# Kernel optimization log

Hardware: AMD Instinct MI355X
Metric: run time of the kernel (lower is better)

## Reference

```python
import jax, jax.numpy as jnp
import numpy as np

N_NODES = 100000
N_EDGES = 1600000
IN_F, HID_F, OUT_F = 128, 128, 128


def setup_inputs() -> dict:
    key = jax.random.key(0)
    ks = jax.random.split(key, 12)
    x = jax.random.normal(ks[0], (N_NODES, IN_F), dtype=jnp.float32)
    src = jax.random.randint(ks[1], (N_EDGES,), 0, N_NODES)
    dst = jax.random.randint(ks[2], (N_EDGES,), 0, N_NODES)
    s = 1.0 / np.sqrt(IN_F)
    W1_self = jax.random.uniform(ks[3], (HID_F, IN_F), minval=-s, maxval=s)
    W1_neigh = jax.random.uniform(ks[4], (HID_F, IN_F), minval=-s, maxval=s)
    b1 = jnp.zeros((HID_F,), jnp.float32)
    s2 = 1.0 / np.sqrt(HID_F)
    W2_self = jax.random.uniform(ks[5], (OUT_F, HID_F), minval=-s2, maxval=s2)
    W2_neigh = jax.random.uniform(ks[6], (OUT_F, HID_F), minval=-s2, maxval=s2)
    b2 = jnp.zeros((OUT_F,), jnp.float32)
    s3 = 1.0 / np.sqrt(OUT_F)
    W3 = jax.random.uniform(ks[7], (OUT_F, OUT_F), minval=-s3, maxval=s3)
    b3 = jax.random.uniform(ks[8], (OUT_F,), minval=-s3, maxval=s3)
    return {"x": x, "src": src, "dst": dst,
            "W1_self": W1_self, "W1_neigh": W1_neigh, "b1": b1,
            "W2_self": W2_self, "W2_neigh": W2_neigh, "b2": b2,
            "W3": W3, "b3": b3}


def _sage_conv(h, src, dst, W_self, W_neigh, b):
    # DGL SAGEConv 'mean': h_neigh = mean over in-neighbors (src -> dst)
    msg = h[src]  # [E, d] irregular gather
    summed = jax.ops.segment_sum(msg, dst, num_segments=N_NODES)  # [N, d]
    deg = jax.ops.segment_sum(jnp.ones((src.shape[0],), h.dtype), dst,
                              num_segments=N_NODES)
    h_neigh = summed / jnp.clip(deg, 1.0)[:, None]
    return h @ W_self.T + h_neigh @ W_neigh.T + b


def reference(x, src, dst, W1_self, W1_neigh, b1, W2_self, W2_neigh, b2, W3, b3):
    h = _sage_conv(x, src, dst, W1_self, W1_neigh, b1)
    h = jax.nn.relu(h)
    h = _sage_conv(h, src, dst, W2_self, W2_neigh, b2)
    return h @ W3.T + b3
```

## Files before the change

### kernel.cpp

```cpp
#include <hip/hip_runtime.h>

#define N_NODES 100000
#define N_EDGES 1600000
#define F 128
#define NB_SCAN ((N_NODES + 1023) / 1024)
#define NSUB 32
#define SUB_NODES (N_NODES / NSUB)
#define BCAP 128
#define PCAP 65536
#define NCHUNK 8
#define NCVT ((N_NODES * F / 8 + 255) / 256)
#define BUCKET_BLOCKS 512
#define PREP_BLOCKS (NCVT + 257)

typedef short short8 __attribute__((ext_vector_type(8)));
typedef float f32x4 __attribute__((ext_vector_type(4)));
typedef unsigned short ushort_t;
typedef ushort_t ushort8 __attribute__((ext_vector_type(8)));

__device__ __forceinline__ ushort_t f2b(float f) {
    union { float f; unsigned u; } v; v.f = f;
    unsigned r = v.u + 0x7fff + ((v.u >> 16) & 1);
    return (ushort_t)(r >> 16);
}


__global__ __launch_bounds__(256) void k_bucket_prep(
        const int* __restrict__ src, const int* __restrict__ dst,
        int2* __restrict__ pairs, int* __restrict__ gcur,
        const float* __restrict__ x, ushort_t* __restrict__ xb,
        const float* __restrict__ W1s, const float* __restrict__ W1n,
        const float* __restrict__ W2s, const float* __restrict__ W2n,
        const float* __restrict__ W3, const float* __restrict__ b2,
        const float* __restrict__ b3,
        ushort_t* __restrict__ wb, float* __restrict__ bc) {
    const int tid = threadIdx.x;

    if (blockIdx.x >= BUCKET_BLOCKS) {
        const int blk = blockIdx.x - BUCKET_BLOCKS;
        if (blk < NCVT) {
            int i = blk * 256 + tid;
            if (i >= N_NODES * F / 8) return;
            const float4* p = reinterpret_cast<const float4*>(x) + (size_t)i * 2;
            float4 a = p[0], b = p[1];
            ushort8 r;
            r[0] = f2b(a.x); r[1] = f2b(a.y); r[2] = f2b(a.z); r[3] = f2b(a.w);
            r[4] = f2b(b.x); r[5] = f2b(b.y); r[6] = f2b(b.z); r[7] = f2b(b.w);
            *reinterpret_cast<ushort8*>(xb + (size_t)i * 8) = r;
            return;
        }
        const int b = blk - NCVT;
        if (b < 128) {
            int g = b * 256 + tid;
            float v = (g < F * F) ? W1s[g] : W1n[g - F * F];
            wb[g] = f2b(v);
        } else if (b < 256) {
            int g = (b - 128) * 256 + tid;
            int m = g >> 14, rem = g & 16383, i = rem >> 7, j = rem & 127;
            const float* __restrict__ W2 = m ? W2n : W2s;
            float s = 0.f;
#pragma unroll 8
            for (int k = 0; k < F; ++k) s += W3[i * F + k] * W2[k * F + j];
            wb[2 * F * F + g] = f2b(s);
        } else if (tid < F) {
            float s = b3[tid];
#pragma unroll 8
            for (int k = 0; k < F; ++k) s += W3[tid * F + k] * b2[k];
            bc[tid] = s;
        }
        return;
    }

    __shared__ int2 lbuf[NSUB * BCAP];
    __shared__ int lcnt[NSUB], fbase[NSUB], fcnt[NSUB];
    if (tid < NSUB) lcnt[tid] = 0;
    __syncthreads();

    for (int base = blockIdx.x * 1024; base < N_EDGES; base += BUCKET_BLOCKS * 1024) {
#pragma unroll
        for (int r = 0; r < 4; ++r) {
            int idx = base + r * 256 + tid;
            if (idx < N_EDGES) {
                int d = dst[idx], s = src[idx];
                int p = d / SUB_NODES;
                int dl = d - p * SUB_NODES;
                int slot = atomicAdd(&lcnt[p], 1);
                if (slot < BCAP) lbuf[p * BCAP + slot] = make_int2(dl, s);
                else {
                    int g = atomicAdd(&gcur[p], 1);
                    pairs[(size_t)p * PCAP + g] = make_int2(dl, s);
                }
            }
        }
        __syncthreads();
        if (tid < NSUB) {
            int c = lcnt[tid]; if (c > BCAP) c = BCAP;
            fcnt[tid] = c;
            fbase[tid] = atomicAdd(&gcur[tid], c);
        }
        __syncthreads();
        for (int p = 0; p < NSUB; ++p) {
            int c = fcnt[p];
            for (int i = tid; i < c; i += 256)
                pairs[(size_t)p * PCAP + fbase[p] + i] = lbuf[p * BCAP + i];
        }
        __syncthreads();
        if (tid < NSUB) lcnt[tid] = 0;
        __syncthreads();
    }
}

__global__ __launch_bounds__(1024) void k_histc(const int2* __restrict__ pairs,
                                                const int* __restrict__ gcur,
                                                int* __restrict__ hists) {
    __shared__ int hc[SUB_NODES];
    const int p = blockIdx.x / NCHUNK;
    const int c = blockIdx.x % NCHUNK;
    for (int i = threadIdx.x; i < SUB_NODES; i += 1024) hc[i] = 0;
    __syncthreads();
    const int n = gcur[p];
    const int chunk = (n + NCHUNK - 1) / NCHUNK;
    const int lo = c * chunk;
    int hi = lo + chunk; if (hi > n) hi = n;
    const int2* __restrict__ sl = pairs + (size_t)p * PCAP;
    for (int i = lo + threadIdx.x; i < hi; i += 1024) atomicAdd(&hc[sl[i].x], 1);
    __syncthreads();
    int* __restrict__ hout = hists + ((size_t)p * NCHUNK + c) * SUB_NODES;
    for (int i = threadIdx.x; i < SUB_NODES; i += 1024) hout[i] = hc[i];
}

__global__ __launch_bounds__(1024) void k_scan1(const int* __restrict__ hists,
                                                int* __restrict__ tmp,
                                                int* __restrict__ bsum) {
    __shared__ int ws[16];
    const int t = threadIdx.x, lane = t & 63, w = t >> 6;
    const int gid = blockIdx.x * 1024 + t;
    int v = 0;
    if (gid < N_NODES) {
        int p = gid / SUB_NODES, i = gid - p * SUB_NODES;
        const int* __restrict__ hp = hists + (size_t)p * NCHUNK * SUB_NODES + i;
#pragma unroll
        for (int c = 0; c < NCHUNK; ++c) v += hp[c * SUB_NODES];
    }
    int x = v;
#pragma unroll
    for (int off = 1; off < 64; off <<= 1) {
        int y = __shfl_up(x, off, 64);
        if (lane >= off) x += y;
    }
    if (lane == 63) ws[w] = x;
    __syncthreads();
    if (w == 0) {
        int s = (lane < 16) ? ws[lane] : 0;
#pragma unroll
        for (int off = 1; off < 16; off <<= 1) {
            int y = __shfl_up(s, off, 64);
            if (lane >= off) s += y;
        }
        if (lane < 16) ws[lane] = s;
    }
    __syncthreads();
    int base = (w == 0) ? 0 : ws[w - 1];
    int incl = base + x;
    if (gid < N_NODES) tmp[gid] = incl;
    if (t == 1023) bsum[blockIdx.x] = incl;
}

__global__ __launch_bounds__(256) void k_scan23(const int* __restrict__ tmp,
                                                const int* __restrict__ bsum,
                                                int* __restrict__ row_ptr) {
    __shared__ int excl[NB_SCAN];
    const int t = threadIdx.x;
    if (t < 64) {
        const int lane = t;
        int v0 = (lane < NB_SCAN) ? bsum[lane] : 0;
        int v1 = (64 + lane < NB_SCAN) ? bsum[64 + lane] : 0;
        int x0 = v0;
#pragma unroll
        for (int off = 1; off < 64; off <<= 1) {
            int y = __shfl_up(x0, off, 64);
            if (lane >= off) x0 += y;
        }
        int tot0 = __shfl(x0, 63, 64);
        int x1 = v1;
#pragma unroll
        for (int off = 1; off < 64; off <<= 1) {
            int y = __shfl_up(x1, off, 64);
            if (lane >= off) x1 += y;
        }
        if (lane < NB_SCAN) excl[lane] = x0 - v0;
        if (64 + lane < NB_SCAN) excl[64 + lane] = tot0 + x1 - v1;
    }
    __syncthreads();
    int gid = blockIdx.x * 256 + t;
    if (gid >= N_NODES) return;
    row_ptr[gid + 1] = excl[gid >> 10] + tmp[gid];
    if (gid == 0) row_ptr[0] = 0;
}

__global__ __launch_bounds__(1024) void k_place2(const int2* __restrict__ pairs,
                                                 const int* __restrict__ gcur,
                                                 const int* __restrict__ row_ptr,
                                                 const int* __restrict__ hists,
                                                 int* __restrict__ col) {
    __shared__ int cur[SUB_NODES];
    const int p = blockIdx.x / NCHUNK;
    const int c = blockIdx.x % NCHUNK;
    const int* __restrict__ hp = hists + (size_t)p * NCHUNK * SUB_NODES;
    for (int i = threadIdx.x; i < SUB_NODES; i += 1024) {
        int s = row_ptr[p * SUB_NODES + i];
        for (int cc = 0; cc < c; ++cc) s += hp[cc * SUB_NODES + i];
        cur[i] = s;
    }
    __syncthreads();
    const int n = gcur[p];
    const int chunk = (n + NCHUNK - 1) / NCHUNK;
    const int lo = c * chunk;
    int hi = lo + chunk; if (hi > n) hi = n;
    const int2* __restrict__ sl = pairs + (size_t)p * PCAP;
    for (int i = lo + threadIdx.x; i < hi; i += 1024) {
        int2 pr = sl[i];
        int pos = atomicAdd(&cur[pr.x], 1);
        col[pos] = pr.y;
    }
}


__global__ __launch_bounds__(256) void k_agg(const ushort_t* __restrict__ h,
                                             const int* __restrict__ row_ptr,
                                             const int* __restrict__ col,
                                             ushort_t* __restrict__ out) {
    int node = (blockIdx.x * blockDim.x + threadIdx.x) >> 6;
    if (node >= N_NODES) return;
    const int lane = threadIdx.x & 63;
    const unsigned loff = (unsigned)lane * 4u;
    const char* __restrict__ hb = reinterpret_cast<const char*>(h);
    const int beg = row_ptr[node], end = row_ptr[node + 1];
    float ax = 0.f, ay = 0.f;
    for (int e = beg; e < end; e += 8) {
        unsigned v[8];
#pragma unroll
        for (int u = 0; u < 8; ++u) {
            int idx = e + u; idx = (idx < end) ? idx : end - 1;
            unsigned s = (unsigned)col[idx];
            v[u] = *reinterpret_cast<const unsigned*>(hb + (size_t)((s << 8) + loff));
        }
#pragma unroll
        for (int u = 0; u < 8; ++u) {
            unsigned vv = (e + u < end) ? v[u] : 0u;
            ax += __uint_as_float(vv << 16);
            ay += __uint_as_float(vv & 0xffff0000u);
        }
    }
    int deg = end - beg;
    float inv = 1.0f / (float)(deg > 0 ? deg : 1);
    unsigned r = ((unsigned)f2b(ax * inv)) | (((unsigned)f2b(ay * inv)) << 16);
    *reinterpret_cast<unsigned*>(out + ((size_t)node << 7) + lane * 2) = r;
}


template <bool RELU, bool F32OUT>
__global__ __launch_bounds__(512) void k_layer(
        const ushort_t* __restrict__ A0, const ushort_t* __restrict__ A1,
        const ushort_t* __restrict__ W0, const ushort_t* __restrict__ W1,
        const float* __restrict__ bias, void* __restrict__ outv) {
    const int t = threadIdx.x;
    const int lane = t & 63;
    const int wid = t >> 6;
    const int wr = wid >> 2;
    const int wc = wid & 3;
    const int node0 = blockIdx.x * 128;
    const int arow = lane & 15;
    const int kgrp = lane >> 4;

    f32x4 acc[4][2];
#pragma unroll
    for (int fr = 0; fr < 4; ++fr)
#pragma unroll
        for (int fc = 0; fc < 2; ++fc) acc[fr][fc] = (f32x4)(0.f);

#pragma unroll
    for (int ph = 0; ph < 2; ++ph) {
        const ushort_t* __restrict__ A = ph ? A1 : A0;
        const ushort_t* __restrict__ W = ph ? W1 : W0;

        short8 bfrag[4][2];
#pragma unroll
        for (int ks = 0; ks < 4; ++ks)
#pragma unroll
            for (int fc = 0; fc < 2; ++fc) {
                int c = wc * 32 + fc * 16 + arow;
                bfrag[ks][fc] = *reinterpret_cast<const short8*>(W + c * F + ks * 32 + kgrp * 8);
            }

#pragma unroll
        for (int ks = 0; ks < 4; ++ks) {
            short8 afrag[4];
#pragma unroll
            for (int fr = 0; fr < 4; ++fr) {
                int r = node0 + wr * 64 + fr * 16 + arow;
                if (r > N_NODES - 1) r = N_NODES - 1;
                afrag[fr] = *reinterpret_cast<const short8*>(A + (size_t)r * F + ks * 32 + kgrp * 8);
            }
#pragma unroll
            for (int fr = 0; fr < 4; ++fr)
#pragma unroll
                for (int fc = 0; fc < 2; ++fc)
                    acc[fr][fc] = __builtin_amdgcn_mfma_f32_16x16x32_bf16(
                        afrag[fr], bfrag[ks][fc], acc[fr][fc], 0, 0, 0);
        }
    }

#pragma unroll
    for (int fr = 0; fr < 4; ++fr)
#pragma unroll
        for (int fc = 0; fc < 2; ++fc) {
            int c = wc * 32 + fc * 16 + (lane & 15);
            float bv = bias[c];
#pragma unroll
            for (int r4 = 0; r4 < 4; ++r4) {
                int row = node0 + wr * 64 + fr * 16 + (lane >> 4) * 4 + r4;
                if (row >= N_NODES) continue;
                float v = acc[fr][fc][r4] + bv;
                if (RELU) v = fmaxf(v, 0.f);
                if (F32OUT)
                    reinterpret_cast<float*>(outv)[(size_t)row * F + c] = v;
                else
                    reinterpret_cast<ushort_t*>(outv)[(size_t)row * F + c] = f2b(v);
            }
        }
}


extern "C" void kernel_launch(void* const* d_in, const int* in_sizes, int n_in,
                              void* d_out, int out_size, void* d_ws, size_t ws_size,
                              hipStream_t stream) {
    const float* x   = (const float*)d_in[0];
    const int*   src = (const int*)d_in[1];
    const int*   dst = (const int*)d_in[2];
    const float* W1s = (const float*)d_in[3];
    const float* W1n = (const float*)d_in[4];
    const float* b1  = (const float*)d_in[5];
    const float* W2s = (const float*)d_in[6];
    const float* W2n = (const float*)d_in[7];
    const float* b2  = (const float*)d_in[8];
    const float* W3  = (const float*)d_in[9];
    const float* b3  = (const float*)d_in[10];
    float* out = (float*)d_out;

    char* p = (char*)d_ws;
    auto align512 = [](size_t v) { return (v + 511) & ~(size_t)511; };
    int* row_ptr = (int*)p;        p += align512((N_NODES + 1) * sizeof(int));
    int* stmp    = (int*)p;        p += align512((size_t)N_NODES * sizeof(int));
    int* bsum    = (int*)p;        p += align512(256 * sizeof(int));
    int* gcur    = (int*)p;        p += align512(NSUB * sizeof(int));
    int* col     = (int*)p;        p += align512((size_t)N_EDGES * sizeof(int));
    ushort_t* wb = (ushort_t*)p;   p += align512((size_t)4 * F * F * sizeof(ushort_t));
    float* bc    = (float*)p;      p += align512(F * sizeof(float));
    ushort_t* xb = (ushort_t*)p;   p += align512((size_t)N_NODES * F * sizeof(ushort_t));
    ushort_t* aggb = (ushort_t*)p; p += align512((size_t)N_NODES * F * sizeof(ushort_t));
    ushort_t* h1b  = (ushort_t*)p; p += align512((size_t)N_NODES * F * sizeof(ushort_t));
    int2* pairs = (int2*)aggb;
    int* hists = (int*)h1b;

    hipMemsetAsync(gcur, 0, NSUB * sizeof(int), stream);
    k_bucket_prep<<<BUCKET_BLOCKS + PREP_BLOCKS, 256, 0, stream>>>(
        src, dst, pairs, gcur, x, xb, W1s, W1n, W2s, W2n, W3, b2, b3, wb, bc);
    k_histc<<<NSUB * NCHUNK, 1024, 0, stream>>>(pairs, gcur, hists);
    k_scan1<<<NB_SCAN, 1024, 0, stream>>>(hists, stmp, bsum);
    k_scan23<<<(N_NODES + 255) / 256, 256, 0, stream>>>(stmp, bsum, row_ptr);
    k_place2<<<NSUB * NCHUNK, 1024, 0, stream>>>(pairs, gcur, row_ptr, hists, col);

    const int agg_grid = (N_NODES + 3) / 4;
    const int gemm_grid = (N_NODES + 127) / 128;

    k_agg<<<agg_grid, 256, 0, stream>>>(xb, row_ptr, col, aggb);
    k_layer<true, false><<<gemm_grid, 512, 0, stream>>>(
        xb, aggb, wb + 0 * F * F, wb + 1 * F * F, b1, h1b);

    k_agg<<<agg_grid, 256, 0, stream>>>(h1b, row_ptr, col, aggb);
    k_layer<false, true><<<gemm_grid, 512, 0, stream>>>(
        h1b, aggb, wb + 2 * F * F, wb + 3 * F * F, bc, out);
}
```

Measured before the change: 302.0 us.

## Fuse CSR scan kernels into placement kernel using per-bucket edge counts

Replaces the two global prefix-scan kernels and the separate placement kernel with one kernel. Each block gets its bucket's base offset by summing the preceding bucket counts (gcur), scans its bucket's histogram locally and then places edges. This removes two kernel launches and the intermediate temp and block-sum buffers. In exchange, every one of the NCHUNK blocks per bucket redundantly re-reads and scans the full bucket histogram.

```diff
diff --git a/kernel.cpp b/kernel.cpp
--- a/kernel.cpp
+++ b/kernel.cpp
@@ -3,7 +3,6 @@
 #define N_NODES 100000
 #define N_EDGES 1600000
 #define F 128
-#define NB_SCAN ((N_NODES + 1023) / 1024)
 #define NSUB 32
 #define SUB_NODES (N_NODES / NSUB)
 #define BCAP 128
@@ -129,20 +128,41 @@
     for (int i = threadIdx.x; i < SUB_NODES; i += 1024) hout[i] = hc[i];
 }
 
-__global__ __launch_bounds__(1024) void k_scan1(const int* __restrict__ hists,
-                                                int* __restrict__ tmp,
-                                                int* __restrict__ bsum) {
+__global__ __launch_bounds__(1024) void k_place3(const int2* __restrict__ pairs,
+                                                 const int* __restrict__ gcur,
+                                                 const int* __restrict__ hists,
+                                                 int* __restrict__ row_ptr,
+                                                 int* __restrict__ col) {
+    __shared__ int cur[SUB_NODES];
     __shared__ int ws[16];
     const int t = threadIdx.x, lane = t & 63, w = t >> 6;
-    const int gid = blockIdx.x * 1024 + t;
-    int v = 0;
-    if (gid < N_NODES) {
-        int p = gid / SUB_NODES, i = gid - p * SUB_NODES;
-        const int* __restrict__ hp = hists + (size_t)p * NCHUNK * SUB_NODES + i;
-#pragma unroll
-        for (int c = 0; c < NCHUNK; ++c) v += hp[c * SUB_NODES];
-    }
-    int x = v;
+    const int p = blockIdx.x / NCHUNK;
+    const int c = blockIdx.x % NCHUNK;
+    const int* __restrict__ hp = hists + (size_t)p * NCHUNK * SUB_NODES;
+
+    int pv = (lane < p) ? gcur[lane] : 0;
+#pragma unroll
+    for (int off = 32; off > 0; off >>= 1) pv += __shfl_xor(pv, off, 64);
+    const int pbase = pv;
+
+    int cnt[4], par[4];
+#pragma unroll
+    for (int j = 0; j < 4; ++j) {
+        int i = t * 4 + j;
+        int full = 0, part = 0;
+        if (i < SUB_NODES) {
+#pragma unroll
+            for (int cc = 0; cc < NCHUNK; ++cc) {
+                int hv = hp[cc * SUB_NODES + i];
+                full += hv;
+                if (cc < c) part += hv;
+            }
+        }
+        cnt[j] = full; par[j] = part;
+    }
+    int lsum = cnt[0] + cnt[1] + cnt[2] + cnt[3];
+
+    int x = lsum;
 #pragma unroll
     for (int off = 1; off < 64; off <<= 1) {
         int y = __shfl_up(x, off, 64);
@@ -160,65 +180,26 @@
         if (lane < 16) ws[lane] = s;
     }
     __syncthreads();
-    int base = (w == 0) ? 0 : ws[w - 1];
-    int incl = base + x;
-    if (gid < N_NODES) tmp[gid] = incl;
-    if (t == 1023) bsum[blockIdx.x] = incl;
-}
-
-__global__ __launch_bounds__(256) void k_scan23(const int* __restrict__ tmp,
-                                                const int* __restrict__ bsum,
-                                                int* __restrict__ row_ptr) {
-    __shared__ int excl[NB_SCAN];
-    const int t = threadIdx.x;
-    if (t < 64) {
-        const int lane = t;
-        int v0 = (lane < NB_SCAN) ? bsum[lane] : 0;
-        int v1 = (64 + lane < NB_SCAN) ? bsum[64 + lane] : 0;
-        int x0 = v0;
-#pragma unroll
-        for (int off = 1; off < 64; off <<= 1) {
-            int y = __shfl_up(x0, off, 64);
-            if (lane >= off) x0 += y;
-        }
-        int tot0 = __shfl(x0, 63, 64);
-        int x1 = v1;
-#pragma unroll
-        for (int off = 1; off < 64; off <<= 1) {
-            int y = __shfl_up(x1, off, 64);
-            if (lane >= off) x1 += y;
-        }
-        if (lane < NB_SCAN) excl[lane] = x0 - v0;
-        if (64 + lane < NB_SCAN) excl[64 + lane] = tot0 + x1 - v1;
-    }
-    __syncthreads();
-    int gid = blockIdx.x * 256 + t;
-    if (gid >= N_NODES) return;
-    row_ptr[gid + 1] = excl[gid >> 10] + tmp[gid];
-    if (gid == 0) row_ptr[0] = 0;
-}
-
-__global__ __launch_bounds__(1024) void k_place2(const int2* __restrict__ pairs,
-                                                 const int* __restrict__ gcur,
-                                                 const int* __restrict__ row_ptr,
-                                                 const int* __restrict__ hists,
-                                                 int* __restrict__ col) {
-    __shared__ int cur[SUB_NODES];
-    const int p = blockIdx.x / NCHUNK;
-    const int c = blockIdx.x % NCHUNK;
-    const int* __restrict__ hp = hists + (size_t)p * NCHUNK * SUB_NODES;
-    for (int i = threadIdx.x; i < SUB_NODES; i += 1024) {
-        int s = row_ptr[p * SUB_NODES + i];
-        for (int cc = 0; cc < c; ++cc) s += hp[cc * SUB_NODES + i];
-        cur[i] = s;
-    }
-    __syncthreads();
+    int run = pbase + ((w == 0) ? 0 : ws[w - 1]) + x - lsum;
+
+#pragma unroll
+    for (int j = 0; j < 4; ++j) {
+        int i = t * 4 + j;
+        if (i < SUB_NODES) {
+            cur[i] = run + par[j];
+            if (c == 0) row_ptr[p * SUB_NODES + i] = run;
+            run += cnt[j];
+        }
+    }
+    if (p == 0 && c == 0 && t == 0) row_ptr[N_NODES] = N_EDGES;
+    __syncthreads();
+
     const int n = gcur[p];
     const int chunk = (n + NCHUNK - 1) / NCHUNK;
     const int lo = c * chunk;
     int hi = lo + chunk; if (hi > n) hi = n;
     const int2* __restrict__ sl = pairs + (size_t)p * PCAP;
-    for (int i = lo + threadIdx.x; i < hi; i += 1024) {
+    for (int i = lo + t; i < hi; i += 1024) {
         int2 pr = sl[i];
         int pos = atomicAdd(&cur[pr.x], 1);
         col[pos] = pr.y;
@@ -351,8 +332,6 @@
     char* p = (char*)d_ws;
     auto align512 = [](size_t v) { return (v + 511) & ~(size_t)511; };
     int* row_ptr = (int*)p;        p += align512((N_NODES + 1) * sizeof(int));
-    int* stmp    = (int*)p;        p += align512((size_t)N_NODES * sizeof(int));
-    int* bsum    = (int*)p;        p += align512(256 * sizeof(int));
     int* gcur    = (int*)p;        p += align512(NSUB * sizeof(int));
     int* col     = (int*)p;        p += align512((size_t)N_EDGES * sizeof(int));
     ushort_t* wb = (ushort_t*)p;   p += align512((size_t)4 * F * F * sizeof(ushort_t));
@@ -367,9 +346,7 @@
     k_bucket_prep<<<BUCKET_BLOCKS + PREP_BLOCKS, 256, 0, stream>>>(
         src, dst, pairs, gcur, x, xb, W1s, W1n, W2s, W2n, W3, b2, b3, wb, bc);
     k_histc<<<NSUB * NCHUNK, 1024, 0, stream>>>(pairs, gcur, hists);
-    k_scan1<<<NB_SCAN, 1024, 0, stream>>>(hists, stmp, bsum);
-    k_scan23<<<(N_NODES + 255) / 256, 256, 0, stream>>>(stmp, bsum, row_ptr);
-    k_place2<<<NSUB * NCHUNK, 1024, 0, stream>>>(pairs, gcur, row_ptr, hists, col);
+    k_place3<<<NSUB * NCHUNK, 1024, 0, stream>>>(pairs, gcur, hists, row_ptr, col);
 
     const int agg_grid = (N_NODES + 3) / 4;
     const int gemm_grid = (N_NODES + 127) / 128;
```

Result: no change. 299.4 us (-0.9%).
